# Optimization experiments

Hardware: AMD Instinct MI355X
Metric: run time of the kernel (lower is better)

The kernel has to match this reference:

```python
import jax, jax.numpy as jnp
import numpy as np

N, E, F, H, G, C = 50000, 800000, 128, 128, 500, 10
L = 3  # num_conv_layers
EPS = 1e-5


def batch_norm(x, g, b):
    # training-mode BatchNorm1d: biased variance, eps=1e-5
    mu = jnp.mean(x, axis=0)
    var = jnp.var(x, axis=0)
    return (x - mu) * jax.lax.rsqrt(var + EPS) * g + b


def gcn_conv(x, W, bias, src, dst, n):
    # x' = D^{-1/2} (A + I) D^{-1/2} (x W) + bias, edge weights = 1
    xw = x @ W
    loop = jnp.arange(n)
    s = jnp.concatenate([src, loop])  # sources incl. self-loops
    d = jnp.concatenate([dst, loop])  # targets incl. self-loops
    w = jnp.ones(s.shape[0], x.dtype)
    deg = jax.ops.segment_sum(w, s, num_segments=n)
    dinv = jnp.where(deg > 0, jax.lax.rsqrt(deg), 0.0)
    norm = dinv[s] * w * dinv[d]
    msg = xw[s] * norm[:, None]  # gather + scale
    out = jax.ops.segment_sum(msg, d, num_segments=n)  # scatter-add
    return out + bias


def setup_inputs() -> dict:
    key = jax.random.key(0)
    ks = jax.random.split(key, 16)
    x = jax.random.normal(ks[0], (N, F), dtype=jnp.float32)
    edge_index = jax.random.randint(ks[1], (2, E), 0, N, dtype=jnp.int64)
    batch = jnp.sort(jax.random.randint(ks[2], (N,), 0, G, dtype=jnp.int64))
    sF = 1.0 / np.sqrt(F)
    sH = 1.0 / np.sqrt(H)
    return {
        "x": x,
        "edge_index": edge_index,
        "batch": batch,
        "bn_feat_g": jnp.ones((F,), jnp.float32),
        "bn_feat_b": jnp.full((F,), 1e-4, jnp.float32),
        "W_feat": jax.random.normal(ks[3], (F, H), jnp.float32) * sF,
        "bns_conv_g": jnp.ones((L, H), jnp.float32),
        "bns_conv_b": jnp.full((L, H), 1e-4, jnp.float32),
        "W_conv": jax.random.normal(ks[4], (L, H, H), jnp.float32) * sH,
        "b_conv": jnp.zeros((L, H), jnp.float32),
        "bn_fc_g": jnp.ones((H,), jnp.float32),
        "bn_fc_b": jnp.full((H,), 1e-4, jnp.float32),
        "W_lin": jax.random.normal(ks[5], (H, H), jnp.float32) * sH,
        "b_lin": jnp.zeros((H,), jnp.float32),
        "bn_hid_g": jnp.ones((H,), jnp.float32),
        "bn_hid_b": jnp.full((H,), 1e-4, jnp.float32),
        "W_cls": jax.random.normal(ks[6], (H, C), jnp.float32) * sH,
        "b_cls": jnp.zeros((C,), jnp.float32),
    }


def reference(x, edge_index, batch, bn_feat_g, bn_feat_b, W_feat,
              bns_conv_g, bns_conv_b, W_conv, b_conv,
              bn_fc_g, bn_fc_b, W_lin, b_lin,
              bn_hid_g, bn_hid_b, W_cls, b_cls):
    src, dst = edge_index[0], edge_index[1]
    h = batch_norm(x, bn_feat_g, bn_feat_b)
    h = jax.nn.relu(h @ W_feat)  # gfn conv: linear only, no bias/propagation
    for i in range(L):
        h = batch_norm(h, bns_conv_g[i], bns_conv_b[i])
        h = jax.nn.relu(gcn_conv(h, W_conv[i], b_conv[i], src, dst, N))
    h = jax.ops.segment_sum(h, batch, num_segments=G)  # global_add_pool
    h = batch_norm(h, bn_fc_g, bn_fc_b)
    h = jax.nn.relu(h @ W_lin + b_lin)
    h = batch_norm(h, bn_hid_g, bn_hid_b)
    logits = h @ W_cls + b_cls
    return jax.nn.log_softmax(logits, axis=-1)
```

## Files before the change

kernel.cpp:

```cpp
#include <hip/hip_runtime.h>

#define NF 128
#define EPS 1e-5f
#define KELL 64
#define HB 64
#define HRANGE 32768
#define BCAP 5120
#define SB 512

typedef unsigned short ushort_t;
typedef unsigned int uint_t;

using bf16x8 = __attribute__((ext_vector_type(8))) short;
using f32x4  = __attribute__((ext_vector_type(4))) float;

static __device__ inline ushort_t f2bf(float f) {
    uint_t u = __float_as_uint(f);
    return (ushort_t)((u + 0x7fffu + ((u >> 16) & 1u)) >> 16);
}


__launch_bounds__(1024)
__global__ void k_prep(const int* __restrict__ ei, uint_t* __restrict__ gcnt,
                       uint_t* __restrict__ bedge, uint_t* __restrict__ hpart,
                       const float* __restrict__ W0, const float* __restrict__ W123,
                       ushort_t* __restrict__ Wp, const float* __restrict__ x,
                       float* __restrict__ stx, int E, int n) {
    __shared__ union {
        struct { uint_t cnt[256]; uint_t cur[256]; uint_t base[256]; } bk;
        uint_t h2[HRANGE / 2];
        struct { float ls[1024]; float lq[1024]; } st;
    } sh;
    const int blk = blockIdx.x;
    const int t = threadIdx.x;

    if (blk < 256) {
        if (t < 256) { sh.bk.cnt[t] = 0; sh.bk.cur[t] = 0; }
        __syncthreads();
        const int chunk = (E + 255) / 256;
        const int e0 = blk * chunk;
        const int e1 = min(e0 + chunk, E);
        for (int e = e0 + t; e < e1; e += 1024)
            atomicAdd(&sh.bk.cnt[ei[E + e] >> 8], 1);
        __syncthreads();
        if (t < 256) {
            uint_t c = sh.bk.cnt[t];
            sh.bk.base[t] = c ? atomicAdd(&gcnt[t], c) : 0u;
        }
        __syncthreads();
        for (int e = e0 + t; e < e1; e += 1024) {
            int s = ei[e], d = ei[E + e];
            int b = d >> 8;
            uint_t pos = sh.bk.base[b] + atomicAdd(&sh.bk.cur[b], 1);
            if (pos < BCAP)
                bedge[((size_t)b << 12) + ((size_t)b << 10) + pos] =
                    ((uint_t)(d & 255) << 16) | (uint_t)s;
        }
    } else if (blk < 320) {
        const int b = blk - 256;
#pragma unroll
        for (int p = 0; p < 2; ++p) {
            int base = p * HRANGE;
            for (int w = t; w < HRANGE / 2; w += 1024) sh.h2[w] = 0;
            __syncthreads();
            for (int e = b * 1024 + t; e < E; e += HB * 1024) {
                unsigned u = (unsigned)(ei[e] - base);
                if (u < HRANGE)
                    atomicAdd(&sh.h2[u >> 1], 1u << ((u & 1) << 4));
            }
            __syncthreads();
            uint_t* dst = hpart + ((size_t)(p * HB + b) << 14);
            for (int w = t; w < HRANGE / 2; w += 1024) dst[w] = sh.h2[w];
            __syncthreads();
        }
    } else if (blk < 322) {
#pragma unroll
        for (int kk = 0; kk < 4; ++kk) {
            int gidx = (blk - 320) * 4096 + kk * 1024 + t;
            int mat = gidx >> 11, idx = gidx & 2047;
            const float* W = (mat == 0) ? W0 : (W123 + (size_t)(mat - 1) * NF * NF);
            int lane = idx & 63, ct = (idx >> 6) & 7, kc = idx >> 9;
            int m = lane & 15, q = lane >> 4;
            ushort_t o[8];
#pragma unroll
            for (int j = 0; j < 8; ++j)
                o[j] = f2bf(W[(kc * 32 + q * 8 + j) * NF + ct * 16 + m]);
            *(uint4*)&Wp[(size_t)gidx * 8] = *(uint4*)o;
        }
    } else {
        const int b = blk - 322;
        const int j = t & 127;
        const int row8 = t >> 7;
        float s = 0.f, q = 0.f;
        for (int r = b * 8 + row8; r < n; r += SB * 8) {
            float v = x[(size_t)r * NF + j];
            s += v; q += v * v;
        }
        sh.st.ls[t] = s; sh.st.lq[t] = q;
        __syncthreads();
        if (t < 128) {
            float ss = 0.f, qq = 0.f;
#pragma unroll
            for (int k = 0; k < 8; ++k) {
                ss += sh.st.ls[t + k * 128];
                qq += sh.st.lq[t + k * 128];
            }
            atomicAdd(&stx[t], ss);
            atomicAdd(&stx[NF + t], qq);
        }
    }
}

__launch_bounds__(256)
__global__ void k_build(const uint_t* __restrict__ gcnt, const uint_t* __restrict__ bedge,
                        const uint_t* __restrict__ hpart, int* __restrict__ ucnt,
                        float* __restrict__ dinv, ushort_t* __restrict__ colx,
                        ushort_t* __restrict__ BbSent, int n) {
    __shared__ ushort_t ell[256][KELL];
    __shared__ uint_t lcnt[256];
    const int b = blockIdx.x, t = threadIdx.x;
    lcnt[t] = 0;
    __syncthreads();
    const int nb = min((int)gcnt[b], BCAP);
    const int node0 = b << 8;
    const uint_t* bsrc = bedge + ((size_t)b << 12) + ((size_t)b << 10);
    for (int e = t; e < nb; e += 256) {
        uint_t pk = bsrc[e];
        int dl = (pk >> 16) & 255;
        uint_t pos = atomicAdd(&lcnt[dl], 1);
        if (pos < KELL - 1) ell[dl][pos] = (ushort_t)(pk & 0xffffu);
    }
    __syncthreads();
    const int i = node0 + t;
    if (i < n) {
        int w = min((int)lcnt[t], KELL - 1);
        ell[t][w] = (ushort_t)i;
        int len = (w + 16) & ~15;
        for (int q = w + 1; q < len; ++q) ell[t][q] = (ushort_t)n;
        ucnt[i] = w;
        int p = i >> 15;
        int u = i & (HRANGE - 1);
        int wd = u >> 1, sh = (u & 1) << 4;
        const uint_t* basep = hpart + ((size_t)(p * HB) << 14) + wd;
        uint_t sum = 0;
#pragma unroll 8
        for (int bb = 0; bb < HB; ++bb) sum += basep[(size_t)bb << 14];
        sum = (sum >> sh) & 0xffffu;
        dinv[i] = rsqrtf((float)sum + 1.0f);
    }
    __syncthreads();
    int nrow = min(n - node0, 256);
    if (nrow > 0) {
        const uint4* src = (const uint4*)&ell[0][0];
        uint4* dst = (uint4*)&colx[(size_t)node0 * KELL];
        int lim = nrow * (KELL * 2 / 16);
        for (int wds = t; wds < lim; wds += 256) dst[wds] = src[wds];
    }
    if (b == 0 && t < 64)
        ((uint_t*)BbSent)[t] = 0;
}


__global__ void bn_stats_bf(const ushort_t* __restrict__ h, float* __restrict__ stats, int n) {
    int j = threadIdx.x & 127;
    int half = threadIdx.x >> 7;
    float s = 0.f, q = 0.f;
    for (int r = blockIdx.x * 2 + half; r < n; r += gridDim.x * 2) {
        float v = __uint_as_float((uint_t)h[(size_t)r * NF + j] << 16);
        s += v;
        q += v * v;
    }
    __shared__ float ls[256], lq[256];
    ls[threadIdx.x] = s; lq[threadIdx.x] = q;
    __syncthreads();
    if (threadIdx.x < 128) {
        atomicAdd(&stats[j], ls[threadIdx.x] + ls[threadIdx.x + 128]);
        atomicAdd(&stats[NF + j], lq[threadIdx.x] + lq[threadIdx.x + 128]);
    }
}


#define HSTRIDE 136

__launch_bounds__(512)
__global__ void gemm_mfma(const void* __restrict__ In, int inbf, const ushort_t* __restrict__ Wp,
                          const float* __restrict__ stats, const float* __restrict__ gW,
                          const float* __restrict__ bB, float inv_n,
                          const float* __restrict__ bias, const float* __restrict__ rowscale,
                          float* __restrict__ out, ushort_t* __restrict__ outb,
                          float* __restrict__ statsOut,
                          int nrows, int relu, int obf) {
    __shared__ union {
        ushort_t hs[64 * HSTRIDE];
        float    ob[32][132];
        ushort_t obu[64][136];
    } shu;
    __shared__ float acs[256];
    __shared__ float cs[128], cq[128];
    const int tid = threadIdx.x;
    const int rb = blockIdx.x * 64;

    if (tid < 128) {
        float mean = stats[tid] * inv_n;
        float var = stats[NF + tid] * inv_n - mean * mean;
        float rstd = rsqrtf(var + EPS);
        float a = gW[tid] * rstd;
        acs[tid] = a;
        acs[NF + tid] = bB[tid] - mean * a;
        cs[tid] = 0.f; cq[tid] = 0.f;
    }
    __syncthreads();
    const float4* ac4 = (const float4*)acs;

#pragma unroll
    for (int p = 0; p < 4; ++p) {
        int idx = p * 512 + tid;
        int r = idx >> 5, k4 = idx & 31;
        int gr = rb + r;
        float4 v = make_float4(0.f, 0.f, 0.f, 0.f);
        if (gr < nrows) {
            if (inbf) {
                uint2 u = *(const uint2*)((const ushort_t*)In + (size_t)gr * NF + k4 * 4);
                v.x = __uint_as_float(u.x << 16);
                v.y = __uint_as_float(u.x & 0xffff0000u);
                v.z = __uint_as_float(u.y << 16);
                v.w = __uint_as_float(u.y & 0xffff0000u);
            } else {
                v = *(const float4*)((const float*)In + (size_t)gr * NF + k4 * 4);
            }
        }
        float4 a4 = ac4[k4], c4 = ac4[32 + k4];
        ushort_t o[4];
        o[0] = f2bf(fmaf(v.x, a4.x, c4.x));
        o[1] = f2bf(fmaf(v.y, a4.y, c4.y));
        o[2] = f2bf(fmaf(v.z, a4.z, c4.z));
        o[3] = f2bf(fmaf(v.w, a4.w, c4.w));
        *(uint2*)&shu.hs[r * HSTRIDE + k4 * 4] = *(uint2*)o;
    }
    __syncthreads();

    const int wave = tid >> 6, lane = tid & 63;
    const int wr = wave & 3;
    const int wc = wave >> 2;
    const int m = lane & 15, q = lane >> 4;
    const ushort_t* arow = &shu.hs[(wr * 16 + m) * HSTRIDE];

    f32x4 acc[4];
#pragma unroll
    for (int ct = 0; ct < 4; ++ct) acc[ct] = (f32x4){0.f, 0.f, 0.f, 0.f};

#pragma unroll
    for (int kc = 0; kc < 4; ++kc) {
        bf16x8 af = *(const bf16x8*)&arow[kc * 32 + q * 8];
        const ushort_t* wp = Wp + kc * 4096 + (wc * 4) * 512 + lane * 8;
#pragma unroll
        for (int ct = 0; ct < 4; ++ct) {
            bf16x8 bfr = *(const bf16x8*)&wp[ct * 512];
            acc[ct] = __builtin_amdgcn_mfma_f32_16x16x32_bf16(af, bfr, acc[ct], 0, 0, 0);
        }
    }

    int grows[4]; float rsv[4]; bool gv[4];
#pragma unroll
    for (int r = 0; r < 4; ++r) {
        grows[r] = rb + wr * 16 + q * 4 + r;
        gv[r] = grows[r] < nrows;
        rsv[r] = (obf && rowscale && gv[r]) ? rowscale[grows[r]] : 1.0f;
    }

    if (statsOut) {
#pragma unroll
        for (int ct = 0; ct < 4; ++ct) {
            int col = (wc * 4 + ct) * 16 + m;
            float bcol = bias ? bias[col] : 0.f;
            float s = 0.f, qq = 0.f;
#pragma unroll
            for (int r = 0; r < 4; ++r) {
                if (gv[r]) {
                    float v = acc[ct][r] + bcol;
                    if (relu) v = fmaxf(v, 0.f);
                    s += v; qq += v * v;
                }
            }
            atomicAdd(&cs[col], s); atomicAdd(&cq[col], qq);
        }
    }

    __syncthreads();

    if (obf) {
#pragma unroll
        for (int ct = 0; ct < 4; ++ct) {
            int col = (wc * 4 + ct) * 16 + m;
            float bcol = bias ? bias[col] : 0.f;
#pragma unroll
            for (int r = 0; r < 4; ++r) {
                int row = wr * 16 + q * 4 + r;
                float v = acc[ct][r] + bcol;
                if (relu) v = fmaxf(v, 0.f);
                shu.obu[row][col] = f2bf(v * rsv[r]);
            }
        }
        __syncthreads();
#pragma unroll
        for (int i = 0; i < 2; ++i) {
            int idx = i * 512 + tid;
            int r = idx >> 4, c8 = idx & 15;
            int grow = rb + r;
            if (grow < nrows)
                *(uint4*)&outb[(size_t)grow * NF + c8 * 8] =
                    *(const uint4*)&shu.obu[r][c8 * 8];
        }
    } else {
#pragma unroll
        for (int h = 0; h < 2; ++h) {
            if ((wr >> 1) == h) {
#pragma unroll
                for (int ct = 0; ct < 4; ++ct) {
                    int col = (wc * 4 + ct) * 16 + m;
                    float bcol = bias ? bias[col] : 0.f;
#pragma unroll
                    for (int r = 0; r < 4; ++r) {
                        int row = (wr & 1) * 16 + q * 4 + r;
                        float v = acc[ct][r] + bcol;
                        if (relu) v = fmaxf(v, 0.f);
                        shu.ob[row][col] = v;
                    }
                }
            }
            __syncthreads();
#pragma unroll
            for (int i = 0; i < 2; ++i) {
                int idx = i * 512 + tid;
                int r = idx >> 5, c4 = idx & 31;
                int grow = rb + h * 32 + r;
                if (grow < nrows)
                    *(float4*)&out[(size_t)grow * NF + c4 * 4] =
                        *(const float4*)&shu.ob[r][c4 * 4];
            }
            __syncthreads();
        }
    }

    if (statsOut) {
        if (tid < 128) {
            atomicAdd(&statsOut[tid], cs[tid]);
            atomicAdd(&statsOut[NF + tid], cq[tid]);
        }
    }
}


__launch_bounds__(256)
__global__ void gemm_bn(const float* __restrict__ Hh, const float* __restrict__ W,
                        const float* __restrict__ stats, const float* __restrict__ gW,
                        const float* __restrict__ bB, float inv_n,
                        const float* __restrict__ bias,
                        float* __restrict__ out, float* __restrict__ statsOut,
                        int nrows, int relu) {
    __shared__ float hsb[64][133];
    __shared__ float acs[256];
    __shared__ float cs[128], cq[128];
    const int tid = threadIdx.x;
    const int tx = tid & 15;
    const int ty = tid >> 4;
    const int rb = blockIdx.x * 64;

    if (tid < 128) {
        float mean = stats[tid] * inv_n;
        float var = stats[NF + tid] * inv_n - mean * mean;
        float rstd = rsqrtf(var + EPS);
        float a = gW[tid] * rstd;
        acs[tid] = a;
        acs[NF + tid] = bB[tid] - mean * a;
        cs[tid] = 0.f; cq[tid] = 0.f;
    }
    __syncthreads();

#pragma unroll 8
    for (int p = 0; p < 32; ++p) {
        int idx = p * 256 + tid;
        int r = idx >> 7, k = idx & 127;
        int gr = rb + r;
        float v = (gr < nrows) ? Hh[(size_t)gr * NF + k] : 0.f;
        hsb[r][k] = fmaf(v, acs[k], acs[NF + k]);
    }
    __syncthreads();

    float acc[4][8];
#pragma unroll
    for (int i = 0; i < 4; ++i)
#pragma unroll
        for (int j = 0; j < 8; ++j) acc[i][j] = 0.f;

    const int c0 = tx * 4, c1 = 64 + tx * 4;
#pragma unroll 4
    for (int k = 0; k < 128; ++k) {
        const float4 b0 = *(const float4*)&W[k * NF + c0];
        const float4 b1 = *(const float4*)&W[k * NF + c1];
#pragma unroll
        for (int i = 0; i < 4; ++i) {
            float a = hsb[ty * 4 + i][k];
            acc[i][0] = fmaf(a, b0.x, acc[i][0]);
            acc[i][1] = fmaf(a, b0.y, acc[i][1]);
            acc[i][2] = fmaf(a, b0.z, acc[i][2]);
            acc[i][3] = fmaf(a, b0.w, acc[i][3]);
            acc[i][4] = fmaf(a, b1.x, acc[i][4]);
            acc[i][5] = fmaf(a, b1.y, acc[i][5]);
            acc[i][6] = fmaf(a, b1.z, acc[i][6]);
            acc[i][7] = fmaf(a, b1.w, acc[i][7]);
        }
    }

    float scol[8], qcol[8];
#pragma unroll
    for (int j = 0; j < 8; ++j) { scol[j] = 0.f; qcol[j] = 0.f; }
#pragma unroll
    for (int i = 0; i < 4; ++i) {
        int gr = rb + ty * 4 + i;
        if (gr < nrows) {
            float o[8];
#pragma unroll
            for (int j = 0; j < 8; ++j) {
                int c = (j < 4) ? (c0 + j) : (c1 + j - 4);
                float v = acc[i][j] + (bias ? bias[c] : 0.f);
                o[j] = relu ? fmaxf(v, 0.f) : v;
                scol[j] += o[j]; qcol[j] += o[j] * o[j];
            }
            *(float4*)&out[(size_t)gr * NF + c0] = make_float4(o[0], o[1], o[2], o[3]);
            *(float4*)&out[(size_t)gr * NF + c1] = make_float4(o[4], o[5], o[6], o[7]);
        }
    }
    if (statsOut) {
#pragma unroll
        for (int j = 0; j < 8; ++j) {
            int c = (j < 4) ? (c0 + j) : (c1 + j - 4);
            atomicAdd(&cs[c], scol[j]);
            atomicAdd(&cq[c], qcol[j]);
        }
        __syncthreads();
        if (tid < 128) {
            atomicAdd(&statsOut[tid], cs[tid]);
            atomicAdd(&statsOut[NF + tid], cq[tid]);
        }
    }
}


#define CVT2(u, a, b) { a = __uint_as_float((u) << 16); b = __uint_as_float((u) & 0xffff0000u); }
#define ACC8(q) { float p0, p1, p2, p3, p4, p5, p6, p7;                          \
    CVT2(q.x, p0, p1) CVT2(q.y, p2, p3) CVT2(q.z, p4, p5) CVT2(q.w, p6, p7)      \
    acc[0] += p0; acc[1] += p1; acc[2] += p2; acc[3] += p3;                      \
    acc[4] += p4; acc[5] += p5; acc[6] += p6; acc[7] += p7; }

__launch_bounds__(256)
__global__ void k_aggregate_bf(const ushort_t* __restrict__ xwb, const int* __restrict__ ucnt,
                               const ushort_t* __restrict__ colx, const float* __restrict__ dinv,
                               const float* __restrict__ bias, float* __restrict__ out,
                               ushort_t* __restrict__ outb, int n) {
    int node = blockIdx.x * 16 + (threadIdx.x >> 4);
    int lane = threadIdx.x & 15;
    if (node >= n) return;
    const uint4* __restrict__ xq = (const uint4*)xwb;
    float acc[8];
#pragma unroll
    for (int j = 0; j < 8; ++j) acc[j] = 0.f;
    int dc = min(ucnt[node], KELL - 1);
    int len = (dc + 16) & ~15;
    int e0 = node * KELL;
    for (int e = e0; e < e0 + len; e += 16) {
        uint4 ia = *(const uint4*)&colx[e];
        uint4 ib = *(const uint4*)&colx[e + 8];
        int i0 = ia.x & 0xffff, i1 = ia.x >> 16;
        int i2 = ia.y & 0xffff, i3 = ia.y >> 16;
        int i4 = ia.z & 0xffff, i5 = ia.z >> 16;
        int i6 = ia.w & 0xffff, i7 = ia.w >> 16;
        int i8 = ib.x & 0xffff, i9 = ib.x >> 16;
        int iA = ib.y & 0xffff, iB = ib.y >> 16;
        int iC = ib.z & 0xffff, iD = ib.z >> 16;
        int iE = ib.w & 0xffff, iF = ib.w >> 16;
        uint4 q0 = xq[(size_t)i0 * 16 + lane];
        uint4 q1 = xq[(size_t)i1 * 16 + lane];
        uint4 q2 = xq[(size_t)i2 * 16 + lane];
        uint4 q3 = xq[(size_t)i3 * 16 + lane];
        uint4 q4 = xq[(size_t)i4 * 16 + lane];
        uint4 q5 = xq[(size_t)i5 * 16 + lane];
        uint4 q6 = xq[(size_t)i6 * 16 + lane];
        uint4 q7 = xq[(size_t)i7 * 16 + lane];
        uint4 q8 = xq[(size_t)i8 * 16 + lane];
        uint4 q9 = xq[(size_t)i9 * 16 + lane];
        uint4 qA = xq[(size_t)iA * 16 + lane];
        uint4 qB = xq[(size_t)iB * 16 + lane];
        uint4 qC = xq[(size_t)iC * 16 + lane];
        uint4 qD = xq[(size_t)iD * 16 + lane];
        uint4 qE = xq[(size_t)iE * 16 + lane];
        uint4 qF = xq[(size_t)iF * 16 + lane];
        ACC8(q0) ACC8(q1) ACC8(q2) ACC8(q3)
        ACC8(q4) ACC8(q5) ACC8(q6) ACC8(q7)
        ACC8(q8) ACC8(q9) ACC8(qA) ACC8(qB)
        ACC8(qC) ACC8(qD) ACC8(qE) ACC8(qF)
    }
    float di = dinv[node];
    float4 b0 = *(const float4*)&bias[lane * 8];
    float4 b1 = *(const float4*)&bias[lane * 8 + 4];
    float4 o0, o1;
    o0.x = fmaxf(fmaf(di, acc[0], b0.x), 0.f);
    o0.y = fmaxf(fmaf(di, acc[1], b0.y), 0.f);
    o0.z = fmaxf(fmaf(di, acc[2], b0.z), 0.f);
    o0.w = fmaxf(fmaf(di, acc[3], b0.w), 0.f);
    o1.x = fmaxf(fmaf(di, acc[4], b1.x), 0.f);
    o1.y = fmaxf(fmaf(di, acc[5], b1.y), 0.f);
    o1.z = fmaxf(fmaf(di, acc[6], b1.z), 0.f);
    o1.w = fmaxf(fmaf(di, acc[7], b1.w), 0.f);
    if (outb) {
        ushort_t ob[8];
        ob[0] = f2bf(o0.x); ob[1] = f2bf(o0.y); ob[2] = f2bf(o0.z); ob[3] = f2bf(o0.w);
        ob[4] = f2bf(o1.x); ob[5] = f2bf(o1.y); ob[6] = f2bf(o1.z); ob[7] = f2bf(o1.w);
        *(uint4*)&outb[(size_t)node * NF + lane * 8] = *(uint4*)ob;
    } else {
        *(float4*)&out[(size_t)node * NF + lane * 8] = o0;
        *(float4*)&out[(size_t)node * NF + lane * 8 + 4] = o1;
    }
}


__global__ void k_pool(const float* __restrict__ h, const int* __restrict__ batch,
                       float* __restrict__ pooled, float* __restrict__ stats, int n) {
    int g = blockIdx.x;
    int t = threadIdx.x;
    int lo = 0, hi = n;
    while (lo < hi) { int m = (lo + hi) >> 1; if (batch[m] < g) lo = m + 1; else hi = m; }
    int start = lo;
    lo = start; hi = n;
    while (lo < hi) { int m = (lo + hi) >> 1; if (batch[m] < g + 1) lo = m + 1; else hi = m; }
    int end = lo;
    float a0 = 0.f, a1 = 0.f, a2 = 0.f, a3 = 0.f;
    int r = start;
    for (; r + 4 <= end; r += 4) {
        a0 += h[(size_t)r * NF + t];
        a1 += h[(size_t)(r + 1) * NF + t];
        a2 += h[(size_t)(r + 2) * NF + t];
        a3 += h[(size_t)(r + 3) * NF + t];
    }
    for (; r < end; ++r) a0 += h[(size_t)r * NF + t];
    float val = (a0 + a1) + (a2 + a3);
    pooled[g * NF + t] = val;
    atomicAdd(&stats[t], val);
    atomicAdd(&stats[NF + t], val * val);
}


__global__ void k_cls(const float* __restrict__ h, const float* __restrict__ stats,
                      const float* __restrict__ gW, const float* __restrict__ bB,
                      float inv_n, const float* __restrict__ Wc,
                      const float* __restrict__ bc, float* __restrict__ out, int C_) {
    __shared__ float hr[128];
    __shared__ float lg[16];
    __shared__ float lse_s;
    int r = blockIdx.x, t = threadIdx.x;
#pragma unroll
    for (int half = 0; half < 2; ++half) {
        int j = t + half * 64;
        float mean = stats[j] * inv_n;
        float var = stats[NF + j] * inv_n - mean * mean;
        float rstd = rsqrtf(var + EPS);
        float a = gW[j] * rstd;
        float c = bB[j] - mean * a;
        hr[j] = fmaf(h[r * NF + j], a, c);
    }
    __syncthreads();
    if (t < C_) {
        float s = bc[t];
        for (int k = 0; k < 128; ++k) s = fmaf(hr[k], Wc[k * C_ + t], s);
        lg[t] = s;
    }
    __syncthreads();
    if (t == 0) {
        float m = -1e30f;
        for (int c = 0; c < C_; ++c) m = fmaxf(m, lg[c]);
        float se = 0.f;
        for (int c = 0; c < C_; ++c) se += expf(lg[c] - m);
        lse_s = m + logf(se);
    }
    __syncthreads();
    if (t < C_) out[r * C_ + t] = lg[t] - lse_s;
}


extern "C" void kernel_launch(void* const* d_in, const int* in_sizes, int n_in,
                              void* d_out, int out_size, void* d_ws, size_t ws_size,
                              hipStream_t stream) {
    const float* x          = (const float*)d_in[0];
    const int*   ei         = (const int*)d_in[1];
    const int*   batch      = (const int*)d_in[2];
    const float* bn_feat_g  = (const float*)d_in[3];
    const float* bn_feat_b  = (const float*)d_in[4];
    const float* W_feat     = (const float*)d_in[5];
    const float* bns_conv_g = (const float*)d_in[6];
    const float* bns_conv_b = (const float*)d_in[7];
    const float* W_conv     = (const float*)d_in[8];
    const float* b_conv     = (const float*)d_in[9];
    const float* bn_fc_g    = (const float*)d_in[10];
    const float* bn_fc_b    = (const float*)d_in[11];
    const float* W_lin      = (const float*)d_in[12];
    const float* b_lin      = (const float*)d_in[13];
    const float* bn_hid_g   = (const float*)d_in[14];
    const float* bn_hid_b   = (const float*)d_in[15];
    const float* W_cls      = (const float*)d_in[16];
    const float* b_cls      = (const float*)d_in[17];
    float* outp = (float*)d_out;

    const int N_ = in_sizes[2];
    const int E_ = in_sizes[1] / 2;
    const int C_ = 10;
    const int G_ = out_size / C_;
    const int NBUCK = (N_ + 255) >> 8;

    char* wsp = (char*)d_ws;
    auto alloc = [&](size_t bytes) {
        void* p = (void*)wsp;
        wsp += (bytes + 255) & ~(size_t)255;
        return p;
    };
    uint_t*   gcnt   = (uint_t*)alloc(256 * 4);
    float*    statsA = (float*)alloc(6 * 256 * 4);
    float*    A      = (float*)alloc((size_t)N_ * NF * 4);
    ushort_t* Ab     = (ushort_t*)alloc((size_t)N_ * NF * 2);
    ushort_t* Bb     = (ushort_t*)alloc((size_t)(N_ + 1) * NF * 2);
    float*    dinv   = (float*)alloc((size_t)N_ * 4);
    int*      ucnt   = (int*)alloc((size_t)N_ * 4);
    uint_t*   bedge  = (uint_t*)alloc((size_t)256 * BCAP * 4);
    ushort_t* colx   = (ushort_t*)alloc((size_t)N_ * KELL * 2);
    uint_t*   hpart  = (uint_t*)alloc((size_t)2 * HB * (HRANGE / 2) * 4);
    ushort_t* Wp     = (ushort_t*)alloc((size_t)4 * NF * NF * 2);
    float*    pooled = (float*)alloc((size_t)G_ * NF * 4);
    float*    y2     = (float*)alloc((size_t)G_ * NF * 4);

    float* st_x  = statsA;
    float* st_f  = statsA + 256;
    float* st_a1 = statsA + 512;
    float* st_a2 = statsA + 768;
    float* st_pl = statsA + 1024;
    float* st_y2 = statsA + 1280;

    int nb_g = (N_ + 63) / 64;

    hipMemsetAsync(gcnt, 0, 1024 + 6 * 256 * 4, stream);

    k_prep<<<322 + SB, 1024, 0, stream>>>(ei, gcnt, bedge, hpart, W_feat, W_conv, Wp,
                                          x, st_x, E_, N_);
    k_build<<<NBUCK, 256, 0, stream>>>(gcnt, bedge, hpart, ucnt, dinv, colx,
                                       Bb + (size_t)N_ * NF, N_);

    gemm_mfma<<<nb_g, 512, 0, stream>>>(x, 0, Wp, st_x, bn_feat_g, bn_feat_b, 1.0f / N_,
                                        nullptr, nullptr, nullptr, Ab, st_f, N_, 1, 1);

    float* st_in[3] = {st_f, st_a1, st_a2};
    float* st_out[3] = {st_a1, st_a2, nullptr};
    for (int l = 0; l < 3; ++l) {
        gemm_mfma<<<nb_g, 512, 0, stream>>>(Ab, 1, Wp + (size_t)(l + 1) * NF * NF,
                                            st_in[l], bns_conv_g + l * NF, bns_conv_b + l * NF,
                                            1.0f / N_, nullptr, dinv, nullptr, Bb, nullptr,
                                            N_, 0, 1);
        if (l < 2) {
            k_aggregate_bf<<<(N_ + 15) / 16, 256, 0, stream>>>(Bb, ucnt, colx, dinv,
                                                               b_conv + l * NF, nullptr, Ab, N_);
            bn_stats_bf<<<512, 256, 0, stream>>>(Ab, st_out[l], N_);
        } else {
            k_aggregate_bf<<<(N_ + 15) / 16, 256, 0, stream>>>(Bb, ucnt, colx, dinv,
                                                               b_conv + l * NF, A, nullptr, N_);
        }
    }

    k_pool<<<G_, 128, 0, stream>>>(A, batch, pooled, st_pl, N_);

    gemm_bn<<<(G_ + 63) / 64, 256, 0, stream>>>(pooled, W_lin, st_pl, bn_fc_g, bn_fc_b,
                                                1.0f / G_, b_lin, y2, st_y2, G_, 1);

    k_cls<<<G_, 64, 0, stream>>>(y2, st_y2, bn_hid_g, bn_hid_b, 1.0f / G_,
                                 W_cls, b_cls, outp, C_);
}
```

Before: 411.7 us.

## Fuse BN statistics into aggregation and keep final layer output in bf16

Aggregation kernel now processes 64 nodes per block and accumulates per-column sum and sum-of-squares, reducing via shuffles and shared memory before atomics, removing the separate bn_stats pass over the activations. The last conv layer writes bf16 instead of fp32 and pooling reads bf16 with vectorized loads, halving that traffic. Fewer blocks with sequential node loops may reduce latency hiding in the gather, and stats now use unrounded values.

```diff
diff --git a/kernel.cpp b/kernel.cpp
--- a/kernel.cpp
+++ b/kernel.cpp
@@ -158,25 +158,6 @@
     }
     if (b == 0 && t < 64)
         ((uint_t*)BbSent)[t] = 0;
-}
-
-
-__global__ void bn_stats_bf(const ushort_t* __restrict__ h, float* __restrict__ stats, int n) {
-    int j = threadIdx.x & 127;
-    int half = threadIdx.x >> 7;
-    float s = 0.f, q = 0.f;
-    for (int r = blockIdx.x * 2 + half; r < n; r += gridDim.x * 2) {
-        float v = __uint_as_float((uint_t)h[(size_t)r * NF + j] << 16);
-        s += v;
-        q += v * v;
-    }
-    __shared__ float ls[256], lq[256];
-    ls[threadIdx.x] = s; lq[threadIdx.x] = q;
-    __syncthreads();
-    if (threadIdx.x < 128) {
-        atomicAdd(&stats[j], ls[threadIdx.x] + ls[threadIdx.x + 128]);
-        atomicAdd(&stats[NF + j], lq[threadIdx.x] + lq[threadIdx.x + 128]);
-    }
 }
 
 
@@ -456,97 +437,140 @@
 __launch_bounds__(256)
 __global__ void k_aggregate_bf(const ushort_t* __restrict__ xwb, const int* __restrict__ ucnt,
                                const ushort_t* __restrict__ colx, const float* __restrict__ dinv,
-                               const float* __restrict__ bias, float* __restrict__ out,
-                               ushort_t* __restrict__ outb, int n) {
-    int node = blockIdx.x * 16 + (threadIdx.x >> 4);
-    int lane = threadIdx.x & 15;
-    if (node >= n) return;
+                               const float* __restrict__ bias, ushort_t* __restrict__ outb,
+                               float* __restrict__ statsOut, int n) {
+    __shared__ float cs[128], cq[128];
+    const int t = threadIdx.x;
+    const int lane = t & 15;
+    if (statsOut && t < 128) { cs[t] = 0.f; cq[t] = 0.f; }
     const uint4* __restrict__ xq = (const uint4*)xwb;
-    float acc[8];
-#pragma unroll
-    for (int j = 0; j < 8; ++j) acc[j] = 0.f;
-    int dc = min(ucnt[node], KELL - 1);
-    int len = (dc + 16) & ~15;
-    int e0 = node * KELL;
-    for (int e = e0; e < e0 + len; e += 16) {
-        uint4 ia = *(const uint4*)&colx[e];
-        uint4 ib = *(const uint4*)&colx[e + 8];
-        int i0 = ia.x & 0xffff, i1 = ia.x >> 16;
-        int i2 = ia.y & 0xffff, i3 = ia.y >> 16;
-        int i4 = ia.z & 0xffff, i5 = ia.z >> 16;
-        int i6 = ia.w & 0xffff, i7 = ia.w >> 16;
-        int i8 = ib.x & 0xffff, i9 = ib.x >> 16;
-        int iA = ib.y & 0xffff, iB = ib.y >> 16;
-        int iC = ib.z & 0xffff, iD = ib.z >> 16;
-        int iE = ib.w & 0xffff, iF = ib.w >> 16;
-        uint4 q0 = xq[(size_t)i0 * 16 + lane];
-        uint4 q1 = xq[(size_t)i1 * 16 + lane];
-        uint4 q2 = xq[(size_t)i2 * 16 + lane];
-        uint4 q3 = xq[(size_t)i3 * 16 + lane];
-        uint4 q4 = xq[(size_t)i4 * 16 + lane];
-        uint4 q5 = xq[(size_t)i5 * 16 + lane];
-        uint4 q6 = xq[(size_t)i6 * 16 + lane];
-        uint4 q7 = xq[(size_t)i7 * 16 + lane];
-        uint4 q8 = xq[(size_t)i8 * 16 + lane];
-        uint4 q9 = xq[(size_t)i9 * 16 + lane];
-        uint4 qA = xq[(size_t)iA * 16 + lane];
-        uint4 qB = xq[(size_t)iB * 16 + lane];
-        uint4 qC = xq[(size_t)iC * 16 + lane];
-        uint4 qD = xq[(size_t)iD * 16 + lane];
-        uint4 qE = xq[(size_t)iE * 16 + lane];
-        uint4 qF = xq[(size_t)iF * 16 + lane];
-        ACC8(q0) ACC8(q1) ACC8(q2) ACC8(q3)
-        ACC8(q4) ACC8(q5) ACC8(q6) ACC8(q7)
-        ACC8(q8) ACC8(q9) ACC8(qA) ACC8(qB)
-        ACC8(qC) ACC8(qD) ACC8(qE) ACC8(qF)
-    }
-    float di = dinv[node];
-    float4 b0 = *(const float4*)&bias[lane * 8];
-    float4 b1 = *(const float4*)&bias[lane * 8 + 4];
-    float4 o0, o1;
-    o0.x = fmaxf(fmaf(di, acc[0], b0.x), 0.f);
-    o0.y = fmaxf(fmaf(di, acc[1], b0.y), 0.f);
-    o0.z = fmaxf(fmaf(di, acc[2], b0.z), 0.f);
-    o0.w = fmaxf(fmaf(di, acc[3], b0.w), 0.f);
-    o1.x = fmaxf(fmaf(di, acc[4], b1.x), 0.f);
-    o1.y = fmaxf(fmaf(di, acc[5], b1.y), 0.f);
-    o1.z = fmaxf(fmaf(di, acc[6], b1.z), 0.f);
-    o1.w = fmaxf(fmaf(di, acc[7], b1.w), 0.f);
-    if (outb) {
-        ushort_t ob[8];
-        ob[0] = f2bf(o0.x); ob[1] = f2bf(o0.y); ob[2] = f2bf(o0.z); ob[3] = f2bf(o0.w);
-        ob[4] = f2bf(o1.x); ob[5] = f2bf(o1.y); ob[6] = f2bf(o1.z); ob[7] = f2bf(o1.w);
-        *(uint4*)&outb[(size_t)node * NF + lane * 8] = *(uint4*)ob;
-    } else {
-        *(float4*)&out[(size_t)node * NF + lane * 8] = o0;
-        *(float4*)&out[(size_t)node * NF + lane * 8 + 4] = o1;
-    }
-}
-
-
-__global__ void k_pool(const float* __restrict__ h, const int* __restrict__ batch,
-                       float* __restrict__ pooled, float* __restrict__ stats, int n) {
+    const float4 b0 = *(const float4*)&bias[lane * 8];
+    const float4 b1 = *(const float4*)&bias[lane * 8 + 4];
+    float s8[8], q8[8];
+#pragma unroll
+    for (int j = 0; j < 8; ++j) { s8[j] = 0.f; q8[j] = 0.f; }
+
+#pragma unroll 1
+    for (int it = 0; it < 4; ++it) {
+        int node = blockIdx.x * 64 + it * 16 + (t >> 4);
+        if (node < n) {
+            float acc[8];
+#pragma unroll
+            for (int j = 0; j < 8; ++j) acc[j] = 0.f;
+            int dc = min(ucnt[node], KELL - 1);
+            int len = (dc + 16) & ~15;
+            int e0 = node * KELL;
+            for (int e = e0; e < e0 + len; e += 16) {
+                uint4 ia = *(const uint4*)&colx[e];
+                uint4 ib = *(const uint4*)&colx[e + 8];
+                int i0 = ia.x & 0xffff, i1 = ia.x >> 16;
+                int i2 = ia.y & 0xffff, i3 = ia.y >> 16;
+                int i4 = ia.z & 0xffff, i5 = ia.z >> 16;
+                int i6 = ia.w & 0xffff, i7 = ia.w >> 16;
+                int i8 = ib.x & 0xffff, i9 = ib.x >> 16;
+                int iA = ib.y & 0xffff, iB = ib.y >> 16;
+                int iC = ib.z & 0xffff, iD = ib.z >> 16;
+                int iE = ib.w & 0xffff, iF = ib.w >> 16;
+                uint4 q0 = xq[(size_t)i0 * 16 + lane];
+                uint4 q1 = xq[(size_t)i1 * 16 + lane];
+                uint4 q2 = xq[(size_t)i2 * 16 + lane];
+                uint4 q3 = xq[(size_t)i3 * 16 + lane];
+                uint4 q4 = xq[(size_t)i4 * 16 + lane];
+                uint4 q5 = xq[(size_t)i5 * 16 + lane];
+                uint4 q6 = xq[(size_t)i6 * 16 + lane];
+                uint4 q7 = xq[(size_t)i7 * 16 + lane];
+                uint4 q8v = xq[(size_t)i8 * 16 + lane];
+                uint4 q9 = xq[(size_t)i9 * 16 + lane];
+                uint4 qA = xq[(size_t)iA * 16 + lane];
+                uint4 qB = xq[(size_t)iB * 16 + lane];
+                uint4 qC = xq[(size_t)iC * 16 + lane];
+                uint4 qD = xq[(size_t)iD * 16 + lane];
+                uint4 qE = xq[(size_t)iE * 16 + lane];
+                uint4 qF = xq[(size_t)iF * 16 + lane];
+                ACC8(q0) ACC8(q1) ACC8(q2) ACC8(q3)
+                ACC8(q4) ACC8(q5) ACC8(q6) ACC8(q7)
+                ACC8(q8v) ACC8(q9) ACC8(qA) ACC8(qB)
+                ACC8(qC) ACC8(qD) ACC8(qE) ACC8(qF)
+            }
+            float di = dinv[node];
+            float o[8];
+            o[0] = fmaxf(fmaf(di, acc[0], b0.x), 0.f);
+            o[1] = fmaxf(fmaf(di, acc[1], b0.y), 0.f);
+            o[2] = fmaxf(fmaf(di, acc[2], b0.z), 0.f);
+            o[3] = fmaxf(fmaf(di, acc[3], b0.w), 0.f);
+            o[4] = fmaxf(fmaf(di, acc[4], b1.x), 0.f);
+            o[5] = fmaxf(fmaf(di, acc[5], b1.y), 0.f);
+            o[6] = fmaxf(fmaf(di, acc[6], b1.z), 0.f);
+            o[7] = fmaxf(fmaf(di, acc[7], b1.w), 0.f);
+            ushort_t ob[8];
+#pragma unroll
+            for (int j = 0; j < 8; ++j) ob[j] = f2bf(o[j]);
+            *(uint4*)&outb[(size_t)node * NF + lane * 8] = *(uint4*)ob;
+            if (statsOut) {
+#pragma unroll
+                for (int j = 0; j < 8; ++j) {
+                    s8[j] += o[j];
+                    q8[j] += o[j] * o[j];
+                }
+            }
+        }
+    }
+
+    if (statsOut) {
+        __syncthreads();
+#pragma unroll
+        for (int j = 0; j < 8; ++j) {
+            float v = s8[j], qv = q8[j];
+            v += __shfl_xor(v, 16); qv += __shfl_xor(qv, 16);
+            v += __shfl_xor(v, 32); qv += __shfl_xor(qv, 32);
+            if ((t & 63) < 16) {
+                atomicAdd(&cs[lane * 8 + j], v);
+                atomicAdd(&cq[lane * 8 + j], qv);
+            }
+        }
+        __syncthreads();
+        if (t < 128) {
+            atomicAdd(&statsOut[t], cs[t]);
+            atomicAdd(&statsOut[NF + t], cq[t]);
+        }
+    }
+}
+
+
+__global__ void k_pool_bf(const ushort_t* __restrict__ h, const int* __restrict__ batch,
+                          float* __restrict__ pooled, float* __restrict__ stats, int n) {
+    __shared__ float ps[8][128];
     int g = blockIdx.x;
     int t = threadIdx.x;
+    int lane = t & 15;
+    int rg = t >> 4;
     int lo = 0, hi = n;
     while (lo < hi) { int m = (lo + hi) >> 1; if (batch[m] < g) lo = m + 1; else hi = m; }
     int start = lo;
     lo = start; hi = n;
     while (lo < hi) { int m = (lo + hi) >> 1; if (batch[m] < g + 1) lo = m + 1; else hi = m; }
     int end = lo;
-    float a0 = 0.f, a1 = 0.f, a2 = 0.f, a3 = 0.f;
-    int r = start;
-    for (; r + 4 <= end; r += 4) {
-        a0 += h[(size_t)r * NF + t];
-        a1 += h[(size_t)(r + 1) * NF + t];
-        a2 += h[(size_t)(r + 2) * NF + t];
-        a3 += h[(size_t)(r + 3) * NF + t];
-    }
-    for (; r < end; ++r) a0 += h[(size_t)r * NF + t];
-    float val = (a0 + a1) + (a2 + a3);
-    pooled[g * NF + t] = val;
-    atomicAdd(&stats[t], val);
-    atomicAdd(&stats[NF + t], val * val);
+    float s[8];
+#pragma unroll
+    for (int j = 0; j < 8; ++j) s[j] = 0.f;
+    for (int r = start + rg; r < end; r += 8) {
+        uint4 u = *(const uint4*)&h[(size_t)r * NF + lane * 8];
+        float p0, p1, p2, p3, p4, p5, p6, p7;
+        CVT2(u.x, p0, p1) CVT2(u.y, p2, p3) CVT2(u.z, p4, p5) CVT2(u.w, p6, p7)
+        s[0] += p0; s[1] += p1; s[2] += p2; s[3] += p3;
+        s[4] += p4; s[5] += p5; s[6] += p6; s[7] += p7;
+    }
+#pragma unroll
+    for (int j = 0; j < 8; ++j) ps[rg][lane * 8 + j] = s[j];
+    __syncthreads();
+    if (t < 128) {
+        float v = 0.f;
+#pragma unroll
+        for (int k = 0; k < 8; ++k) v += ps[k][t];
+        pooled[g * NF + t] = v;
+        atomicAdd(&stats[t], v);
+        atomicAdd(&stats[NF + t], v * v);
+    }
 }
 
 
@@ -624,7 +648,6 @@
     };
     uint_t*   gcnt   = (uint_t*)alloc(256 * 4);
     float*    statsA = (float*)alloc(6 * 256 * 4);
-    float*    A      = (float*)alloc((size_t)N_ * NF * 4);
     ushort_t* Ab     = (ushort_t*)alloc((size_t)N_ * NF * 2);
     ushort_t* Bb     = (ushort_t*)alloc((size_t)(N_ + 1) * NF * 2);
     float*    dinv   = (float*)alloc((size_t)N_ * 4);
@@ -644,6 +667,7 @@
     float* st_y2 = statsA + 1280;
 
     int nb_g = (N_ + 63) / 64;
+    int nb_ag = (N_ + 63) / 64;
 
     hipMemsetAsync(gcnt, 0, 1024 + 6 * 256 * 4, stream);
 
@@ -662,17 +686,11 @@
                                             st_in[l], bns_conv_g + l * NF, bns_conv_b + l * NF,
                                             1.0f / N_, nullptr, dinv, nullptr, Bb, nullptr,
                                             N_, 0, 1);
-        if (l < 2) {
-            k_aggregate_bf<<<(N_ + 15) / 16, 256, 0, stream>>>(Bb, ucnt, colx, dinv,
-                                                               b_conv + l * NF, nullptr, Ab, N_);
-            bn_stats_bf<<<512, 256, 0, stream>>>(Ab, st_out[l], N_);
-        } else {
-            k_aggregate_bf<<<(N_ + 15) / 16, 256, 0, stream>>>(Bb, ucnt, colx, dinv,
-                                                               b_conv + l * NF, A, nullptr, N_);
-        }
-    }
-
-    k_pool<<<G_, 128, 0, stream>>>(A, batch, pooled, st_pl, N_);
+        k_aggregate_bf<<<nb_ag, 256, 0, stream>>>(Bb, ucnt, colx, dinv,
+                                                  b_conv + l * NF, Ab, st_out[l], N_);
+    }
+
+    k_pool_bf<<<G_, 128, 0, stream>>>(Ab, batch, pooled, st_pl, N_);
 
     gemm_bn<<<(G_ + 63) / 64, 256, 0, stream>>>(pooled, W_lin, st_pl, bn_fc_g, bn_fc_b,
                                                 1.0f / G_, b_lin, y2, st_y2, G_, 1);
```

Result: no change. 408.9 us (-0.7%).
